# Kernel optimization log

Hardware: AMD Instinct MI355X
Metric: run time of the kernel (lower is better)

## Reference

```python
import jax, jax.numpy as jnp
import numpy as np

B, T, D, HS = 4, 4096, 1024, 64


def setup_inputs() -> dict:
    key = jax.random.key(0)
    k1, k2, k3 = jax.random.split(key, 3)
    x = jax.random.normal(k1, (B, T, D), dtype=jnp.float32)
    # Linear(n_embd, head_size, bias=False) weights: [head_size, n_embd]
    Wk = jax.random.normal(k2, (HS, D), dtype=jnp.float32) * (D ** -0.5)
    Wv = jax.random.normal(k3, (HS, D), dtype=jnp.float32) * (D ** -0.5)
    return {"x": x, "Wk": Wk, "Wv": Wv}


def reference(x, Wk, Wv):
    # Faithful to source: q = self.value(x) (query proj is dead code), so q and v
    # share the value projection.
    k = jnp.einsum('btd,hd->bth', x, Wk)   # [B,T,HS]
    qv = jnp.einsum('btd,hd->bth', x, Wv)  # [B,T,HS]; serves as both q and v
    scale = k.shape[-1] ** -0.5
    scores = jnp.einsum('bth,bsh->bts', qv, k) * scale  # [B,T,T]
    causal = jnp.tril(jnp.ones((T, T), dtype=bool))
    scores = jnp.where(causal, scores, -jnp.inf)
    weights = jax.nn.softmax(scores, axis=-1)
    out = jnp.einsum('bts,bsh->bth', weights, qv)  # [B,T,HS]
    return out
```

## Files before the change

### kernel.cpp

```cpp
#include <hip/hip_runtime.h>
#include <hip/hip_bf16.h>

typedef __bf16 bf16;
typedef __attribute__((ext_vector_type(4))) __bf16 bf16x4;
typedef __attribute__((ext_vector_type(8))) __bf16 bf16x8;
typedef __attribute__((ext_vector_type(4))) float f32x4;
typedef __attribute__((ext_vector_type(4))) short s16x4;

#define T_SEQ 4096
#define D_EMB 1024
#define HS 64

#if __has_builtin(__builtin_amdgcn_mfma_f32_16x16x16bf16_1k)
#define MFMA16_OK 1
#else
#define MFMA16_OK 0
#endif

__device__ __forceinline__ float fexp2(float x) {
#if __has_builtin(__builtin_amdgcn_exp2f)
    return __builtin_amdgcn_exp2f(x);
#else
    return exp2f(x);
#endif
}

#if MFMA16_OK
__device__ __forceinline__ s16x4 bc4(bf16x4 v) {
    return __builtin_bit_cast(s16x4, v);
}
#endif

__global__ __launch_bounds__(256) void wcast_kernel(
    const float* __restrict__ Wk, const float* __restrict__ Wv,
    bf16* __restrict__ wbf)
{
    const int t = blockIdx.x * 256 + threadIdx.x;
    const int base = t * 8;
    const float* src = (base < 65536) ? (Wk + base) : (Wv + base - 65536);
    float4 f0 = *(const float4*)(src);
    float4 f1 = *(const float4*)(src + 4);
    bf16x8 o = {(__bf16)f0.x, (__bf16)f0.y, (__bf16)f0.z, (__bf16)f0.w,
                (__bf16)f1.x, (__bf16)f1.y, (__bf16)f1.z, (__bf16)f1.w};
    *(bf16x8*)(wbf + base) = o;
}

__global__ __launch_bounds__(256, 2) void proj_kernel(
    const float* __restrict__ x,
    const bf16* __restrict__ wbf,
    bf16* __restrict__ kmat,
    bf16* __restrict__ qvmat,
    bf16* __restrict__ qvT)
{
    __shared__ bf16 xs[32][72];
    __shared__ bf16 wsh[128][72];
    __shared__ bf16 vt[64][40];

    const int tid  = threadIdx.x;
    const int lane = tid & 63;
    const int wave = tid >> 6;
    const int col  = lane & 15;
    const int quad = lane >> 4;
    const int rowbase = blockIdx.x * 32;

    f32x4 acc[2][2];
#pragma unroll
    for (int mt = 0; mt < 2; ++mt)
#pragma unroll
        for (int nt = 0; nt < 2; ++nt) acc[mt][nt] = {0.f, 0.f, 0.f, 0.f};

    float4 xn[2];
    bf16x8 wn[4];
    {
#pragma unroll
        for (int p = 0; p < 2; ++p) {
            const int idx = p * 256 + tid;
            const int xr  = idx >> 4;
            const int c4  = (idx & 15) * 4;
            xn[p] = *(const float4*)(x + (size_t)(rowbase + xr) * D_EMB + c4);
        }
#pragma unroll
        for (int p = 0; p < 4; ++p) {
            const int idx = p * 256 + tid;
            const int wr  = idx >> 3;
            const int off = (idx & 7) * 8;
            wn[p] = *(const bf16x8*)(wbf + (size_t)wr * D_EMB + off);
        }
    }

#pragma unroll 1
    for (int c = 0; c < 16; ++c) {
#pragma unroll
        for (int p = 0; p < 2; ++p) {
            const int idx = p * 256 + tid;
            const int xr  = idx >> 4;
            const int c4  = (idx & 15) * 4;
            bf16x4 v = {(__bf16)xn[p].x, (__bf16)xn[p].y,
                        (__bf16)xn[p].z, (__bf16)xn[p].w};
            *(bf16x4*)&xs[xr][c4] = v;
        }
#pragma unroll
        for (int p = 0; p < 4; ++p) {
            const int idx = p * 256 + tid;
            const int wr  = idx >> 3;
            const int off = (idx & 7) * 8;
            *(bf16x8*)&wsh[wr][off] = wn[p];
        }
        __syncthreads();

        if (c < 15) {
            const int k0 = (c + 1) * 64;
#pragma unroll
            for (int p = 0; p < 2; ++p) {
                const int idx = p * 256 + tid;
                const int xr  = idx >> 4;
                const int c4  = (idx & 15) * 4;
                xn[p] = *(const float4*)(x + (size_t)(rowbase + xr) * D_EMB + k0 + c4);
            }
#pragma unroll
            for (int p = 0; p < 4; ++p) {
                const int idx = p * 256 + tid;
                const int wr  = idx >> 3;
                const int off = (idx & 7) * 8;
                wn[p] = *(const bf16x8*)(wbf + (size_t)wr * D_EMB + k0 + off);
            }
        }

#pragma unroll
        for (int s = 0; s < 2; ++s) {
            bf16x8 af[2];
#pragma unroll
            for (int mt = 0; mt < 2; ++mt)
                af[mt] = *(const bf16x8*)&xs[mt * 16 + col][s * 32 + quad * 8];
            bf16x8 bfr[2];
#pragma unroll
            for (int nt = 0; nt < 2; ++nt)
                bfr[nt] = *(const bf16x8*)&wsh[wave * 32 + nt * 16 + col][s * 32 + quad * 8];
#pragma unroll
            for (int mt = 0; mt < 2; ++mt)
#pragma unroll
                for (int nt = 0; nt < 2; ++nt)
                    acc[mt][nt] = __builtin_amdgcn_mfma_f32_16x16x32_bf16(
                        af[mt], bfr[nt], acc[mt][nt], 0, 0, 0);
        }
        __syncthreads();
    }

#pragma unroll
    for (int mt = 0; mt < 2; ++mt)
#pragma unroll
        for (int nt = 0; nt < 2; ++nt) {
            const int gcol = wave * 32 + nt * 16 + col;
#pragma unroll
            for (int r = 0; r < 4; ++r) {
                const int grow = rowbase + mt * 16 + quad * 4 + r;
                const int ltt  = mt * 16 + quad * 4 + r;
                bf16 bv = (bf16)acc[mt][nt][r];
                if (gcol < 64) {
                    kmat[(size_t)grow * HS + gcol] = bv;
                } else {
                    qvmat[(size_t)grow * HS + (gcol - 64)] = bv;
                    vt[gcol - 64][ltt] = bv;
                }
            }
        }
    __syncthreads();

    {
        const int h   = tid >> 2;
        const int seg = (tid & 3) * 8;
        bf16x8 v = *(const bf16x8*)&vt[h][seg];
        const int bb  = rowbase >> 12;
        const int tt0 = (rowbase & (T_SEQ - 1)) + seg;
        *(bf16x8*)(qvT + ((size_t)bb * HS + h) * T_SEQ + tt0) = v;
    }
}

__global__ __launch_bounds__(256, 4) void attn_kernel(
    const bf16* __restrict__ kmat,
    const bf16* __restrict__ qvmat,
    const bf16* __restrict__ qvT,
    float* __restrict__ out,
    float* __restrict__ o_parts,
    float* __restrict__ l_parts)
{
    __shared__ bf16 Kt[64][72];
    __shared__ bf16 Vt[64][72];
#if !MFMA16_OK
    __shared__ bf16 plds[4][16][40];
#endif

    const int tid  = threadIdx.x;
    const int lane = tid & 63;
    const int wave = tid >> 6;
    const int col  = lane & 15;
    const int quad = lane >> 4;

    const int b = blockIdx.x / 288;
    const int r = 287 - (blockIdx.x - b * 288);
    int a = 0;
    while (4 * (a + 1) * (a + 2) <= r) ++a;
    const int rr = r - 4 * a * (a + 1);
    const int m  = rr / (a + 1);
    const int jc = rr - m * (a + 1);
    const int qb = 8 * a + m;

    const int cbeg  = jc * 8;
    const int nctot = qb + 1;
    const int cend  = (nctot < cbeg + 8) ? nctot : cbeg + 8;

    const bf16* qvb = qvmat + (size_t)b * T_SEQ * HS;
    const bf16* kb  = kmat  + (size_t)b * T_SEQ * HS;
    const bf16* vTb = qvT   + (size_t)b * HS * T_SEQ;

    const int q0 = qb * 64 + wave * 16;

    bf16x8 qf0 = *(const bf16x8*)(qvb + (size_t)(q0 + col) * HS + quad * 8);
    bf16x8 qf1 = *(const bf16x8*)(qvb + (size_t)(q0 + col) * HS + 32 + quad * 8);

    f32x4 o[4];
#pragma unroll
    for (int h = 0; h < 4; ++h) o[h] = {0.f, 0.f, 0.f, 0.f};
    float lsum = 0.f;

    const float sc = 0.125f * 1.44269504088896f;

    bf16x8 kn[2], vn[2];
    {
        const int kc = cbeg * 64;
#pragma unroll
        for (int it = 0; it < 2; ++it) {
            const int idx = it * 256 + tid;
            const int kr  = idx >> 3;
            const int off = (idx & 7) * 8;
            kn[it] = *(const bf16x8*)(kb + (size_t)kc * HS + idx * 8);
            vn[it] = *(const bf16x8*)(vTb + (size_t)kr * T_SEQ + kc + off);
        }
    }

#pragma unroll 1
    for (int c = cbeg; c < cend; ++c) {
#pragma unroll
        for (int it = 0; it < 2; ++it) {
            const int idx = it * 256 + tid;
            const int kr  = idx >> 3;
            const int off = (idx & 7) * 8;
            *(bf16x8*)&Kt[kr][off] = kn[it];
            *(bf16x8*)&Vt[kr][off] = vn[it];
        }
        __syncthreads();

        if (c + 1 < cend) {
            const int kcn = (c + 1) * 64;
#pragma unroll
            for (int it = 0; it < 2; ++it) {
                const int idx = it * 256 + tid;
                const int kr  = idx >> 3;
                const int off = (idx & 7) * 8;
                kn[it] = *(const bf16x8*)(kb + (size_t)kcn * HS + idx * 8);
                vn[it] = *(const bf16x8*)(vTb + (size_t)kr * T_SEQ + kcn + off);
            }
        }

        const int kc = c * 64;
#pragma unroll
        for (int st = 0; st < 2; ++st) {
            const int gk = kc + 32 * st;
            if (gk > q0 + 15) break;

            bf16x8 b0 = *(const bf16x8*)&Kt[32 * st + col][quad * 8];
            bf16x8 b1 = *(const bf16x8*)&Kt[32 * st + col][32 + quad * 8];

            float p0[4], p1[4];
            {
                f32x4 a4 = {0.f, 0.f, 0.f, 0.f};
                a4 = __builtin_amdgcn_mfma_f32_16x16x32_bf16(b0, qf0, a4, 0, 0, 0);
                a4 = __builtin_amdgcn_mfma_f32_16x16x32_bf16(b1, qf1, a4, 0, 0, 0);
#pragma unroll
                for (int i = 0; i < 4; ++i) p0[i] = fexp2(fmaf(a4[i], sc, -24.f));
            }
            const bool do1 = (gk + 16 <= q0 + 15);
            if (do1) {
                bf16x8 b2 = *(const bf16x8*)&Kt[32 * st + 16 + col][quad * 8];
                bf16x8 b3 = *(const bf16x8*)&Kt[32 * st + 16 + col][32 + quad * 8];
                f32x4 a4 = {0.f, 0.f, 0.f, 0.f};
                a4 = __builtin_amdgcn_mfma_f32_16x16x32_bf16(b2, qf0, a4, 0, 0, 0);
                a4 = __builtin_amdgcn_mfma_f32_16x16x32_bf16(b3, qf1, a4, 0, 0, 0);
#pragma unroll
                for (int i = 0; i < 4; ++i) p1[i] = fexp2(fmaf(a4[i], sc, -24.f));
            } else {
#pragma unroll
                for (int i = 0; i < 4; ++i) p1[i] = 0.f;
            }

            if (gk + 31 > q0) {
#pragma unroll
                for (int i = 0; i < 4; ++i)
                    if (gk + quad * 4 + i > q0 + col) p0[i] = 0.f;
                if (do1) {
#pragma unroll
                    for (int i = 0; i < 4; ++i)
                        if (gk + 16 + quad * 4 + i > q0 + col) p1[i] = 0.f;
                }
            }

            lsum += (p0[0] + p0[1]) + (p0[2] + p0[3]);
            if (do1) lsum += (p1[0] + p1[1]) + (p1[2] + p1[3]);

#if MFMA16_OK
            bf16x4 pa0 = {(bf16)p0[0], (bf16)p0[1], (bf16)p0[2], (bf16)p0[3]};
            s16x4 pa0s = bc4(pa0);
#pragma unroll
            for (int h = 0; h < 4; ++h) {
                bf16x4 vb = *(const bf16x4*)&Vt[h * 16 + col][32 * st + quad * 4];
                o[h] = __builtin_amdgcn_mfma_f32_16x16x16bf16_1k(
                    pa0s, bc4(vb), o[h], 0, 0, 0);
            }
            if (do1) {
                bf16x4 pa1 = {(bf16)p1[0], (bf16)p1[1], (bf16)p1[2], (bf16)p1[3]};
                s16x4 pa1s = bc4(pa1);
#pragma unroll
                for (int h = 0; h < 4; ++h) {
                    bf16x4 vb = *(const bf16x4*)&Vt[h * 16 + col][32 * st + 16 + quad * 4];
                    o[h] = __builtin_amdgcn_mfma_f32_16x16x16bf16_1k(
                        pa1s, bc4(vb), o[h], 0, 0, 0);
                }
            }
#else
            bf16x4 w0 = {(bf16)p0[0], (bf16)p0[1], (bf16)p0[2], (bf16)p0[3]};
            bf16x4 w1 = {(bf16)p1[0], (bf16)p1[1], (bf16)p1[2], (bf16)p1[3]};
            *(bf16x4*)&plds[wave][col][quad * 4]      = w0;
            *(bf16x4*)&plds[wave][col][16 + quad * 4] = w1;
            bf16x8 pa = *(const bf16x8*)&plds[wave][col][quad * 8];
#pragma unroll
            for (int h = 0; h < 4; ++h) {
                bf16x8 vb = *(const bf16x8*)&Vt[h * 16 + col][32 * st + quad * 8];
                o[h] = __builtin_amdgcn_mfma_f32_16x16x32_bf16(pa, vb, o[h], 0, 0, 0);
            }
#endif
        }
        __syncthreads();
    }

    lsum += __shfl_xor(lsum, 16, 64);
    lsum += __shfl_xor(lsum, 32, 64);
    if (quad == 0)
        l_parts[(size_t)jc * 16384 + (size_t)b * T_SEQ + q0 + col] = lsum;

    const size_t rowbase = (size_t)b * T_SEQ + q0 + quad * 4;
    float* dst = (jc == 0) ? out : (o_parts + (size_t)(jc - 1) * 16384 * HS);
#pragma unroll
    for (int h = 0; h < 4; ++h)
#pragma unroll
        for (int i = 0; i < 4; ++i)
            dst[(rowbase + i) * HS + h * 16 + col] = o[h][i];
}

__global__ __launch_bounds__(256) void norm_kernel(
    float* __restrict__ out,
    const float* __restrict__ o_parts,
    const float* __restrict__ l_parts)
{
    const int i   = blockIdx.x * 256 + threadIdx.x;
    const int row = i >> 6;
    const int qb  = (row & 4095) >> 6;
    const int nj  = (qb >> 3) + 1;

    float s = out[i];
    float L = l_parts[row];
    for (int j = 1; j < nj; ++j) {
        s += o_parts[(size_t)(j - 1) * 1048576 + i];
        L += l_parts[(size_t)j * 16384 + row];
    }
    out[i] = s / L;
}

extern "C" void kernel_launch(void* const* d_in, const int* in_sizes, int n_in,
                              void* d_out, int out_size, void* d_ws, size_t ws_size,
                              hipStream_t stream) {
    const float* x  = (const float*)d_in[0];
    const float* Wk = (const float*)d_in[1];
    const float* Wv = (const float*)d_in[2];
    float* out = (float*)d_out;

    bf16* ws    = (bf16*)d_ws;
    bf16* wbf   = ws;
    bf16* kmat  = ws + (size_t)128 * 1024;
    bf16* qvmat = kmat + (size_t)16384 * 64;
    bf16* qvT   = qvmat + (size_t)16384 * 64;
    float* o_parts = (float*)(qvT + (size_t)16384 * 64);
    float* l_parts = o_parts + (size_t)7 * 16384 * 64;

    wcast_kernel<<<64, 256, 0, stream>>>(Wk, Wv, wbf);
    proj_kernel<<<512, 256, 0, stream>>>(x, wbf, kmat, qvmat, qvT);
    attn_kernel<<<1152, 256, 0, stream>>>(kmat, qvmat, qvT, out, o_parts, l_parts);
    norm_kernel<<<4096, 256, 0, stream>>>(out, o_parts, l_parts);
}
```

Baseline: 137.4 us.

## Process two query tiles per block to reuse K/V LDS tiles

Each attention block now handles two 64-row query tiles, 64 rows apart, and runs both against the same K/V chunk staged in LDS. This halves the K/V loads and LDS staging per query row. The KV split-chunk size changes from 8 to 6 chunks, the block-to-work mapping is rebuilt, and the launch bound drops to 3 blocks per CU to make room for the doubled accumulators. In exchange the kernel uses more registers, has fewer blocks, and writes more partial outputs for the norm kernel to reduce.

```diff
diff --git a/kernel.cpp b/kernel.cpp
--- a/kernel.cpp
+++ b/kernel.cpp
@@ -176,7 +176,7 @@
     }
 }
 
-__global__ __launch_bounds__(256, 4) void attn_kernel(
+__global__ __launch_bounds__(256, 3) void attn_kernel(
     const bf16* __restrict__ kmat,
     const bf16* __restrict__ qvmat,
     const bf16* __restrict__ qvT,
@@ -196,32 +196,35 @@
     const int col  = lane & 15;
     const int quad = lane >> 4;
 
-    const int b = blockIdx.x / 288;
-    const int r = 287 - (blockIdx.x - b * 288);
-    int a = 0;
-    while (4 * (a + 1) * (a + 2) <= r) ++a;
-    const int rr = r - 4 * a * (a + 1);
-    const int m  = rr / (a + 1);
-    const int jc = rr - m * (a + 1);
-    const int qb = 8 * a + m;
-
-    const int cbeg  = jc * 8;
-    const int nctot = qb + 1;
-    const int cend  = (nctot < cbeg + 8) ? nctot : cbeg + 8;
+    const int b = blockIdx.x / 187;
+    int r = blockIdx.x - b * 187;
+    int qb2 = 31, jc = 0;
+#pragma unroll 1
+    for (int q = 31; q >= 0; --q) {
+        const int nj = (2 * q + 7) / 6;
+        if (r < nj) { qb2 = q; jc = r; break; }
+        r -= nj;
+    }
+    const int nctot = 2 * qb2 + 2;
+    const int cbeg  = jc * 6;
+    const int cend  = (nctot < cbeg + 6) ? nctot : cbeg + 6;
 
     const bf16* qvb = qvmat + (size_t)b * T_SEQ * HS;
     const bf16* kb  = kmat  + (size_t)b * T_SEQ * HS;
     const bf16* vTb = qvT   + (size_t)b * HS * T_SEQ;
 
-    const int q0 = qb * 64 + wave * 16;
-
-    bf16x8 qf0 = *(const bf16x8*)(qvb + (size_t)(q0 + col) * HS + quad * 8);
-    bf16x8 qf1 = *(const bf16x8*)(qvb + (size_t)(q0 + col) * HS + 32 + quad * 8);
-
-    f32x4 o[4];
-#pragma unroll
-    for (int h = 0; h < 4; ++h) o[h] = {0.f, 0.f, 0.f, 0.f};
-    float lsum = 0.f;
+    const int q0 = qb2 * 128 + wave * 16;
+    const int q1 = q0 + 64;
+
+    bf16x8 qf0a = *(const bf16x8*)(qvb + (size_t)(q0 + col) * HS + quad * 8);
+    bf16x8 qf0b = *(const bf16x8*)(qvb + (size_t)(q0 + col) * HS + 32 + quad * 8);
+    bf16x8 qf1a = *(const bf16x8*)(qvb + (size_t)(q1 + col) * HS + quad * 8);
+    bf16x8 qf1b = *(const bf16x8*)(qvb + (size_t)(q1 + col) * HS + 32 + quad * 8);
+
+    f32x4 o0[4], o1[4];
+#pragma unroll
+    for (int h = 0; h < 4; ++h) { o0[h] = {0.f, 0.f, 0.f, 0.f}; o1[h] = {0.f, 0.f, 0.f, 0.f}; }
+    float lsum0 = 0.f, lsum1 = 0.f;
 
     const float sc = 0.125f * 1.44269504088896f;
 
@@ -263,97 +266,179 @@
         }
 
         const int kc = c * 64;
+#if MFMA16_OK
+#pragma unroll
+        for (int ks = 0; ks < 4; ++ks) {
+            const int gk = kc + 16 * ks;
+            if (gk > q1 + 15) break;
+
+            bf16x8 ka = *(const bf16x8*)&Kt[16 * ks + col][quad * 8];
+            bf16x8 kbf = *(const bf16x8*)&Kt[16 * ks + col][32 + quad * 8];
+
+            float p1v[4];
+            {
+                f32x4 a4 = {0.f, 0.f, 0.f, 0.f};
+                a4 = __builtin_amdgcn_mfma_f32_16x16x32_bf16(ka,  qf1a, a4, 0, 0, 0);
+                a4 = __builtin_amdgcn_mfma_f32_16x16x32_bf16(kbf, qf1b, a4, 0, 0, 0);
+#pragma unroll
+                for (int i = 0; i < 4; ++i) p1v[i] = fexp2(fmaf(a4[i], sc, -24.f));
+            }
+            if (gk + 15 > q1) {
+#pragma unroll
+                for (int i = 0; i < 4; ++i)
+                    if (gk + quad * 4 + i > q1 + col) p1v[i] = 0.f;
+            }
+            lsum1 += (p1v[0] + p1v[1]) + (p1v[2] + p1v[3]);
+
+            const bool g0 = (gk <= q0 + 15);
+            float p0v[4];
+            if (g0) {
+                f32x4 a4 = {0.f, 0.f, 0.f, 0.f};
+                a4 = __builtin_amdgcn_mfma_f32_16x16x32_bf16(ka,  qf0a, a4, 0, 0, 0);
+                a4 = __builtin_amdgcn_mfma_f32_16x16x32_bf16(kbf, qf0b, a4, 0, 0, 0);
+#pragma unroll
+                for (int i = 0; i < 4; ++i) p0v[i] = fexp2(fmaf(a4[i], sc, -24.f));
+                if (gk + 15 > q0) {
+#pragma unroll
+                    for (int i = 0; i < 4; ++i)
+                        if (gk + quad * 4 + i > q0 + col) p0v[i] = 0.f;
+                }
+                lsum0 += (p0v[0] + p0v[1]) + (p0v[2] + p0v[3]);
+            }
+
+            bf16x4 pb1 = {(bf16)p1v[0], (bf16)p1v[1], (bf16)p1v[2], (bf16)p1v[3]};
+            s16x4 pa1s = bc4(pb1);
+            s16x4 pa0s;
+            if (g0) {
+                bf16x4 pb0 = {(bf16)p0v[0], (bf16)p0v[1], (bf16)p0v[2], (bf16)p0v[3]};
+                pa0s = bc4(pb0);
+            }
+#pragma unroll
+            for (int h = 0; h < 4; ++h) {
+                bf16x4 vb = *(const bf16x4*)&Vt[h * 16 + col][16 * ks + quad * 4];
+                s16x4 vbs = bc4(vb);
+                o1[h] = __builtin_amdgcn_mfma_f32_16x16x16bf16_1k(pa1s, vbs, o1[h], 0, 0, 0);
+                if (g0)
+                    o0[h] = __builtin_amdgcn_mfma_f32_16x16x16bf16_1k(pa0s, vbs, o0[h], 0, 0, 0);
+            }
+        }
+#else
 #pragma unroll
         for (int st = 0; st < 2; ++st) {
             const int gk = kc + 32 * st;
-            if (gk > q0 + 15) break;
+            if (gk > q1 + 15) break;
 
             bf16x8 b0 = *(const bf16x8*)&Kt[32 * st + col][quad * 8];
             bf16x8 b1 = *(const bf16x8*)&Kt[32 * st + col][32 + quad * 8];
-
-            float p0[4], p1[4];
+            const bool t1 = (gk + 16 <= q1 + 15);
+            bf16x8 b2, b3;
+            if (t1) {
+                b2 = *(const bf16x8*)&Kt[32 * st + 16 + col][quad * 8];
+                b3 = *(const bf16x8*)&Kt[32 * st + 16 + col][32 + quad * 8];
+            }
+
+            float pA[4], pB[4];
             {
                 f32x4 a4 = {0.f, 0.f, 0.f, 0.f};
-                a4 = __builtin_amdgcn_mfma_f32_16x16x32_bf16(b0, qf0, a4, 0, 0, 0);
-                a4 = __builtin_amdgcn_mfma_f32_16x16x32_bf16(b1, qf1, a4, 0, 0, 0);
-#pragma unroll
-                for (int i = 0; i < 4; ++i) p0[i] = fexp2(fmaf(a4[i], sc, -24.f));
-            }
-            const bool do1 = (gk + 16 <= q0 + 15);
-            if (do1) {
-                bf16x8 b2 = *(const bf16x8*)&Kt[32 * st + 16 + col][quad * 8];
-                bf16x8 b3 = *(const bf16x8*)&Kt[32 * st + 16 + col][32 + quad * 8];
+                a4 = __builtin_amdgcn_mfma_f32_16x16x32_bf16(b0, qf1a, a4, 0, 0, 0);
+                a4 = __builtin_amdgcn_mfma_f32_16x16x32_bf16(b1, qf1b, a4, 0, 0, 0);
+#pragma unroll
+                for (int i = 0; i < 4; ++i) pA[i] = fexp2(fmaf(a4[i], sc, -24.f));
+            }
+            if (t1) {
                 f32x4 a4 = {0.f, 0.f, 0.f, 0.f};
-                a4 = __builtin_amdgcn_mfma_f32_16x16x32_bf16(b2, qf0, a4, 0, 0, 0);
-                a4 = __builtin_amdgcn_mfma_f32_16x16x32_bf16(b3, qf1, a4, 0, 0, 0);
-#pragma unroll
-                for (int i = 0; i < 4; ++i) p1[i] = fexp2(fmaf(a4[i], sc, -24.f));
+                a4 = __builtin_amdgcn_mfma_f32_16x16x32_bf16(b2, qf1a, a4, 0, 0, 0);
+                a4 = __builtin_amdgcn_mfma_f32_16x16x32_bf16(b3, qf1b, a4, 0, 0, 0);
+#pragma unroll
+                for (int i = 0; i < 4; ++i) pB[i] = fexp2(fmaf(a4[i], sc, -24.f));
             } else {
 #pragma unroll
-                for (int i = 0; i < 4; ++i) p1[i] = 0.f;
-            }
-
-            if (gk + 31 > q0) {
-#pragma unroll
-                for (int i = 0; i < 4; ++i)
-                    if (gk + quad * 4 + i > q0 + col) p0[i] = 0.f;
-                if (do1) {
-#pragma unroll
-                    for (int i = 0; i < 4; ++i)
-                        if (gk + 16 + quad * 4 + i > q0 + col) p1[i] = 0.f;
-                }
-            }
-
-            lsum += (p0[0] + p0[1]) + (p0[2] + p0[3]);
-            if (do1) lsum += (p1[0] + p1[1]) + (p1[2] + p1[3]);
-
-#if MFMA16_OK
-            bf16x4 pa0 = {(bf16)p0[0], (bf16)p0[1], (bf16)p0[2], (bf16)p0[3]};
-            s16x4 pa0s = bc4(pa0);
-#pragma unroll
-            for (int h = 0; h < 4; ++h) {
-                bf16x4 vb = *(const bf16x4*)&Vt[h * 16 + col][32 * st + quad * 4];
-                o[h] = __builtin_amdgcn_mfma_f32_16x16x16bf16_1k(
-                    pa0s, bc4(vb), o[h], 0, 0, 0);
-            }
-            if (do1) {
-                bf16x4 pa1 = {(bf16)p1[0], (bf16)p1[1], (bf16)p1[2], (bf16)p1[3]};
-                s16x4 pa1s = bc4(pa1);
-#pragma unroll
-                for (int h = 0; h < 4; ++h) {
-                    bf16x4 vb = *(const bf16x4*)&Vt[h * 16 + col][32 * st + 16 + quad * 4];
-                    o[h] = __builtin_amdgcn_mfma_f32_16x16x16bf16_1k(
-                        pa1s, bc4(vb), o[h], 0, 0, 0);
-                }
-            }
-#else
-            bf16x4 w0 = {(bf16)p0[0], (bf16)p0[1], (bf16)p0[2], (bf16)p0[3]};
-            bf16x4 w1 = {(bf16)p1[0], (bf16)p1[1], (bf16)p1[2], (bf16)p1[3]};
-            *(bf16x4*)&plds[wave][col][quad * 4]      = w0;
-            *(bf16x4*)&plds[wave][col][16 + quad * 4] = w1;
-            bf16x8 pa = *(const bf16x8*)&plds[wave][col][quad * 8];
+                for (int i = 0; i < 4; ++i) pB[i] = 0.f;
+            }
+            if (gk + 31 > q1) {
+#pragma unroll
+                for (int i = 0; i < 4; ++i) {
+                    if (gk + quad * 4 + i > q1 + col) pA[i] = 0.f;
+                    if (t1 && gk + 16 + quad * 4 + i > q1 + col) pB[i] = 0.f;
+                }
+            }
+            lsum1 += (pA[0] + pA[1]) + (pA[2] + pA[3]) + (pB[0] + pB[1]) + (pB[2] + pB[3]);
+            {
+                bf16x4 w0 = {(bf16)pA[0], (bf16)pA[1], (bf16)pA[2], (bf16)pA[3]};
+                bf16x4 w1 = {(bf16)pB[0], (bf16)pB[1], (bf16)pB[2], (bf16)pB[3]};
+                *(bf16x4*)&plds[wave][col][quad * 4]      = w0;
+                *(bf16x4*)&plds[wave][col][16 + quad * 4] = w1;
+            }
+            bf16x8 pa1 = *(const bf16x8*)&plds[wave][col][quad * 8];
+
+            const bool g0 = (gk <= q0 + 15);
+            bf16x8 pa0;
+            if (g0) {
+                float qA[4], qB[4];
+                {
+                    f32x4 a4 = {0.f, 0.f, 0.f, 0.f};
+                    a4 = __builtin_amdgcn_mfma_f32_16x16x32_bf16(b0, qf0a, a4, 0, 0, 0);
+                    a4 = __builtin_amdgcn_mfma_f32_16x16x32_bf16(b1, qf0b, a4, 0, 0, 0);
+#pragma unroll
+                    for (int i = 0; i < 4; ++i) qA[i] = fexp2(fmaf(a4[i], sc, -24.f));
+                }
+                const bool t0 = (gk + 16 <= q0 + 15);
+                if (t0) {
+                    f32x4 a4 = {0.f, 0.f, 0.f, 0.f};
+                    a4 = __builtin_amdgcn_mfma_f32_16x16x32_bf16(b2, qf0a, a4, 0, 0, 0);
+                    a4 = __builtin_amdgcn_mfma_f32_16x16x32_bf16(b3, qf0b, a4, 0, 0, 0);
+#pragma unroll
+                    for (int i = 0; i < 4; ++i) qB[i] = fexp2(fmaf(a4[i], sc, -24.f));
+                } else {
+#pragma unroll
+                    for (int i = 0; i < 4; ++i) qB[i] = 0.f;
+                }
+                if (gk + 31 > q0) {
+#pragma unroll
+                    for (int i = 0; i < 4; ++i) {
+                        if (gk + quad * 4 + i > q0 + col) qA[i] = 0.f;
+                        if (t0 && gk + 16 + quad * 4 + i > q0 + col) qB[i] = 0.f;
+                    }
+                }
+                lsum0 += (qA[0] + qA[1]) + (qA[2] + qA[3]) + (qB[0] + qB[1]) + (qB[2] + qB[3]);
+                bf16x4 w0 = {(bf16)qA[0], (bf16)qA[1], (bf16)qA[2], (bf16)qA[3]};
+                bf16x4 w1 = {(bf16)qB[0], (bf16)qB[1], (bf16)qB[2], (bf16)qB[3]};
+                *(bf16x4*)&plds[wave][col][quad * 4]      = w0;
+                *(bf16x4*)&plds[wave][col][16 + quad * 4] = w1;
+                pa0 = *(const bf16x8*)&plds[wave][col][quad * 8];
+            }
+
 #pragma unroll
             for (int h = 0; h < 4; ++h) {
                 bf16x8 vb = *(const bf16x8*)&Vt[h * 16 + col][32 * st + quad * 8];
-                o[h] = __builtin_amdgcn_mfma_f32_16x16x32_bf16(pa, vb, o[h], 0, 0, 0);
-            }
+                o1[h] = __builtin_amdgcn_mfma_f32_16x16x32_bf16(pa1, vb, o1[h], 0, 0, 0);
+                if (g0)
+                    o0[h] = __builtin_amdgcn_mfma_f32_16x16x32_bf16(pa0, vb, o0[h], 0, 0, 0);
+            }
+        }
 #endif
-        }
         __syncthreads();
     }
 
-    lsum += __shfl_xor(lsum, 16, 64);
-    lsum += __shfl_xor(lsum, 32, 64);
-    if (quad == 0)
-        l_parts[(size_t)jc * 16384 + (size_t)b * T_SEQ + q0 + col] = lsum;
-
-    const size_t rowbase = (size_t)b * T_SEQ + q0 + quad * 4;
+    lsum0 += __shfl_xor(lsum0, 16, 64);
+    lsum0 += __shfl_xor(lsum0, 32, 64);
+    lsum1 += __shfl_xor(lsum1, 16, 64);
+    lsum1 += __shfl_xor(lsum1, 32, 64);
+    if (quad == 0) {
+        l_parts[(size_t)jc * 16384 + (size_t)b * T_SEQ + q0 + col] = lsum0;
+        l_parts[(size_t)jc * 16384 + (size_t)b * T_SEQ + q1 + col] = lsum1;
+    }
+
     float* dst = (jc == 0) ? out : (o_parts + (size_t)(jc - 1) * 16384 * HS);
+    const size_t rb0 = (size_t)b * T_SEQ + q0 + quad * 4;
+    const size_t rb1 = (size_t)b * T_SEQ + q1 + quad * 4;
 #pragma unroll
     for (int h = 0; h < 4; ++h)
 #pragma unroll
-        for (int i = 0; i < 4; ++i)
-            dst[(rowbase + i) * HS + h * 16 + col] = o[h][i];
+        for (int i = 0; i < 4; ++i) {
+            dst[(rb0 + i) * HS + h * 16 + col] = o0[h][i];
+            dst[(rb1 + i) * HS + h * 16 + col] = o1[h][i];
+        }
 }
 
 __global__ __launch_bounds__(256) void norm_kernel(
@@ -363,8 +448,8 @@
 {
     const int i   = blockIdx.x * 256 + threadIdx.x;
     const int row = i >> 6;
-    const int qb  = (row & 4095) >> 6;
-    const int nj  = (qb >> 3) + 1;
+    const int qb2 = (row & 4095) >> 7;
+    const int nj  = (2 * qb2 + 7) / 6;
 
     float s = out[i];
     float L = l_parts[row];
@@ -389,10 +474,10 @@
     bf16* qvmat = kmat + (size_t)16384 * 64;
     bf16* qvT   = qvmat + (size_t)16384 * 64;
     float* o_parts = (float*)(qvT + (size_t)16384 * 64);
-    float* l_parts = o_parts + (size_t)7 * 16384 * 64;
+    float* l_parts = o_parts + (size_t)10 * 16384 * 64;
 
     wcast_kernel<<<64, 256, 0, stream>>>(Wk, Wv, wbf);
     proj_kernel<<<512, 256, 0, stream>>>(x, wbf, kmat, qvmat, qvT);
-    attn_kernel<<<1152, 256, 0, stream>>>(kmat, qvmat, qvT, out, o_parts, l_parts);
+    attn_kernel<<<748, 256, 0, stream>>>(kmat, qvmat, qvT, out, o_parts, l_parts);
     norm_kernel<<<4096, 256, 0, stream>>>(out, o_parts, l_parts);
 }
```

After: 157.7 us. +14.8%, slower.
